# Kernel optimization log

Measured on AMD Instinct MI355X. Metric: run time of the kernel, lower is better.

The kernel has to match this reference:

```python
import jax, jax.numpy as jnp
import numpy as np

HEAD_SIZE = 64
N_EMBD = 1024

def setup_inputs() -> dict:
    key = jax.random.key(0)
    ks = jax.random.split(key, 7)
    B, T = 4, 4096
    s = 1.0 / np.sqrt(N_EMBD)
    return {
        "x": jax.random.normal(ks[0], (B, T, N_EMBD), dtype=jnp.float32),
        "Wq": jax.random.normal(ks[1], (N_EMBD, HEAD_SIZE), dtype=jnp.float32) * s,
        "bq": jnp.zeros((HEAD_SIZE,), dtype=jnp.float32),
        "Wk": jax.random.normal(ks[2], (N_EMBD, HEAD_SIZE), dtype=jnp.float32) * s,
        "bk": jnp.zeros((HEAD_SIZE,), dtype=jnp.float32),
        "Wv": jax.random.normal(ks[3], (N_EMBD, HEAD_SIZE), dtype=jnp.float32) * s,
        "bv": jnp.zeros((HEAD_SIZE,), dtype=jnp.float32),
    }

def reference(x, Wq, bq, Wk, bk, Wv, bv):
    # q,k,v: [B,T,H]
    q = x @ Wq + bq
    k = x @ Wk + bk
    v = x @ Wv + bv
    scale = jnp.asarray(HEAD_SIZE, x.dtype) ** -0.5
    att = jnp.einsum("bth,bsh->bts", q, k) * scale  # [B,T,T]
    att = jax.nn.softmax(att, axis=-1)
    # dropout with p=0.0 is identity (eval-mode reference)
    return jnp.einsum("bts,bsh->bth", att, v)
```

## Files before the change

kernel.cpp:

```cpp
#include <hip/hip_runtime.h>
#include <hip/hip_bf16.h>
#include <cmath>

#define BATCH 4
#define TLEN  4096
#define CEMB  1024
#define HEAD  64
#define NROWS (BATCH * TLEN)

typedef __bf16 bf16;
typedef __attribute__((ext_vector_type(8))) __bf16 bf16x8;
typedef __attribute__((ext_vector_type(4))) __bf16 bf16x4;
typedef __attribute__((ext_vector_type(4))) float f32x4;
typedef __attribute__((ext_vector_type(16))) float f32x16;
typedef __attribute__((ext_vector_type(4))) unsigned u32x4;

#define QSCALE 0.1803368801111204f

static __device__ __forceinline__ f32x4 mfma16(bf16x8 a, bf16x8 b, f32x4 c) {
    return __builtin_amdgcn_mfma_f32_16x16x32_bf16(a, b, c, 0, 0, 0);
}
static __device__ __forceinline__ f32x16 mfma32(bf16x8 a, bf16x8 b, f32x16 c) {
    return __builtin_amdgcn_mfma_f32_32x32x16_bf16(a, b, c, 0, 0, 0);
}
static __device__ __forceinline__ unsigned cvt_pk_bf16(float lo, float hi) {
    unsigned r;
    asm("v_cvt_pk_bf16_f32 %0, %1, %2" : "=v"(r) : "v"(lo), "v"(hi));
    return r;
}

static __device__ __forceinline__ void async_ld16(const void* g, void* l) {
    __builtin_amdgcn_global_load_lds(
        (const __attribute__((address_space(1))) void*)g,
        (__attribute__((address_space(3))) void*)l, 16, 0, 0);
}

__global__ __launch_bounds__(256) void pack_w(
    const float* __restrict__ Wq, const float* __restrict__ Wk,
    const float* __restrict__ Wv, bf16* __restrict__ Wt)
{
    const int n = blockIdx.x;
    const int which = n >> 6, h = n & 63;
    const float* W = which == 0 ? Wq : (which == 1 ? Wk : Wv);
    const float s = which == 0 ? QSCALE : 1.0f;
    for (int k = threadIdx.x; k < CEMB; k += 256)
        Wt[(size_t)n * CEMB + k] = (bf16)(W[(size_t)k * HEAD + h] * s);
}

__global__ __launch_bounds__(256, 2) void qkv(
    const float* __restrict__ x, const bf16* __restrict__ Wt,
    const float* __restrict__ bq, const float* __restrict__ bk,
    const float* __restrict__ bv,
    bf16* __restrict__ qb, bf16* __restrict__ kb, bf16* __restrict__ vT)
{
    __shared__ __align__(16) float Xsh[2][2][32][64];

    const int tid  = threadIdx.x;
    const int lane = tid & 63;
    const int wvid = tid >> 6;
    const int quad = lane >> 4;
    const int col  = lane & 15;
    const int row0 = blockIdx.x * 32;

    const float* xblk = x + (size_t)row0 * CEMB;
    const bf16* wrow[3];
    #pragma unroll
    for (int j = 0; j < 3; ++j)
        wrow[j] = Wt + (size_t)((wvid * 3 + j) * 16 + col) * CEMB + quad * 8;

    const int sr = lane >> 4;
    const int ss = lane & 15;
    auto stage = [&](int ci, int bufi) {
        #pragma unroll
        for (int h2 = 0; h2 < 2; ++h2)
            #pragma unroll
            for (int j = 0; j < 2; ++j) {
                const int r = wvid * 8 + j * 4 + sr;
                const int c = ss ^ (r & 7);
                async_ld16(xblk + (size_t)r * CEMB + ci * 128 + h2 * 64 + c * 4,
                           &Xsh[bufi][h2][wvid * 8 + j * 4][0]);
            }
    };

    f32x4 acc[2][3] = {};
    const int c7 = col & 7;

    stage(0, 0);
    int buf = 0;
    for (int ci = 0; ci < 8; ++ci) {
        __syncthreads();
        if (ci + 1 < 8) stage(ci + 1, buf ^ 1);

        #pragma unroll
        for (int kk = 0; kk < 4; ++kk) {
            const int h  = ci * 4 + kk;
            const int hf = kk >> 1;
            const int kl = kk & 1;
            bf16x8 Bv[3];
            #pragma unroll
            for (int j = 0; j < 3; ++j)
                Bv[j] = *(const bf16x8*)(wrow[j] + h * 32);
            #pragma unroll
            for (int rt = 0; rt < 2; ++rt) {
                const int r = rt * 16 + col;
                const int g0 = kl * 8 + quad * 2;
                float4 a0 = *(const float4*)&Xsh[buf][hf][r][(g0 ^ c7) * 4];
                float4 a1 = *(const float4*)&Xsh[buf][hf][r][((g0 + 1) ^ c7) * 4];
                bf16x8 af;
                af[0]=(bf16)a0.x; af[1]=(bf16)a0.y; af[2]=(bf16)a0.z; af[3]=(bf16)a0.w;
                af[4]=(bf16)a1.x; af[5]=(bf16)a1.y; af[6]=(bf16)a1.z; af[7]=(bf16)a1.w;
                #pragma unroll
                for (int j = 0; j < 3; ++j)
                    acc[rt][j] = mfma16(af, Bv[j], acc[rt][j]);
            }
        }
        buf ^= 1;
    }

    const float* bias[3] = {bq, bk, bv};
    #pragma unroll
    for (int j = 0; j < 3; ++j) {
        const int jg = wvid * 3 + j;
        const int which = jg >> 2;
        const int h = (jg & 3) * 16 + col;
        float bb = bias[which][h];
        if (which == 0) bb *= QSCALE;
        #pragma unroll
        for (int rt = 0; rt < 2; ++rt) {
            if (which < 2) {
                bf16* dst = which == 0 ? qb : kb;
                #pragma unroll
                for (int r = 0; r < 4; ++r) {
                    const int trow = row0 + rt * 16 + quad * 4 + r;
                    dst[(size_t)trow * HEAD + h] = (bf16)(acc[rt][j][r] + bb);
                }
            } else {
                bf16x4 pv;
                #pragma unroll
                for (int r = 0; r < 4; ++r) pv[r] = (bf16)(acc[rt][j][r] + bb);
                const int trow0 = row0 + rt * 16 + quad * 4;
                const int bb_   = trow0 >> 12;
                const int tt    = trow0 & (TLEN - 1);
                *(bf16x4*)(vT + ((size_t)(bb_ * HEAD + h)) * TLEN + tt) = pv;
            }
        }
    }
}

__global__ __launch_bounds__(256, 2) void attn(
    const bf16* __restrict__ qb, const bf16* __restrict__ kb,
    const bf16* __restrict__ vT,
    bf16* __restrict__ opart, float* __restrict__ lpart,
    float* __restrict__ out, int nsplit, int lg2S)
{
    __shared__ __align__(16) bf16 Ksh[2][64][64];
    __shared__ __align__(16) bf16 Vsh[2][64][64];

    const int tid  = threadIdx.x;
    const int lane = tid & 63;
    const int wvid = tid >> 6;
    const int l31  = lane & 31;
    const int b5   = lane >> 5;

    int b, sp, qtile;
    {
        const int id = blockIdx.x;
        if (nsplit >= 2) {
            const int cpx = (BATCH << lg2S) >> 3;
            const int idx = id >> 3;
            const int combo = (id & 7) * cpx + (idx >> 4);
            qtile = idx & 15;
            b = combo >> lg2S;
            sp = combo & (nsplit - 1);
        } else {
            qtile = id & 15; b = id >> 4; sp = 0;
        }
    }
    const int q0 = qtile * 256 + wvid * 64;
    const size_t rowbase = (size_t)b * TLEN + q0;

    bf16x8 qf[2][4];
    #pragma unroll
    for (int qt = 0; qt < 2; ++qt)
        #pragma unroll
        for (int m = 0; m < 4; ++m)
            qf[qt][m] = *(const bf16x8*)
                (qb + (rowbase + qt * 32 + l31) * HEAD + m * 16 + b5 * 8);

    const bf16* kbB = kb + (size_t)b * TLEN * HEAD;
    const bf16* vTB = vT + (size_t)b * HEAD * TLEN;

    f32x16 o[2][2] = {};
    float lsum[2] = {0.f, 0.f};

    const int slen = TLEN >> lg2S;
    const int sbeg = sp * slen;
    const int nch  = slen / 64;

    const int r8 = lane >> 3;
    const int s8 = lane & 7;
    auto stage = [&](int s0, int bufi) {
        #pragma unroll
        for (int j = 0; j < 2; ++j) {
            const int r = wvid * 16 + j * 8 + r8;
            const int c = s8 ^ (r & 7);
            async_ld16(kbB + (size_t)(s0 + r) * HEAD + c * 8,
                       &Ksh[bufi][wvid * 16 + j * 8][0]);
            async_ld16(vTB + (size_t)r * TLEN + s0 + c * 8,
                       &Vsh[bufi][wvid * 16 + j * 8][0]);
        }
    };

    stage(sbeg, 0);
    int buf = 0;
    for (int ci = 0; ci < nch; ++ci) {
        __syncthreads();
        if (ci + 1 < nch) stage(sbeg + (ci + 1) * 64, buf ^ 1);

        #pragma unroll
        for (int kt = 0; kt < 2; ++kt) {
            const int kr = kt * 32 + l31;
            const int k7 = kr & 7;
            bf16x8 kf[4];
            #pragma unroll
            for (int m = 0; m < 4; ++m)
                kf[m] = *(const bf16x8*)&Ksh[buf][kr][((2 * m + b5) ^ k7) * 8];

            bf16x8 pb[2][2];
            #pragma unroll
            for (int qt = 0; qt < 2; ++qt) {
                f32x16 st = {};
                #pragma unroll
                for (int m = 0; m < 4; ++m)
                    st = mfma32(kf[m], qf[qt][m], st);
                float e[16];
                #pragma unroll
                for (int r = 0; r < 16; ++r)
                    e[r] = __builtin_amdgcn_exp2f(st[r]);
                float t0 = (e[0] + e[1]) + (e[2] + e[3]);
                float t1 = (e[4] + e[5]) + (e[6] + e[7]);
                float t2 = (e[8] + e[9]) + (e[10] + e[11]);
                float t3 = (e[12] + e[13]) + (e[14] + e[15]);
                lsum[qt] += (t0 + t1) + (t2 + t3);
                unsigned w[8];
                #pragma unroll
                for (int s = 0; s < 8; ++s)
                    w[s] = cvt_pk_bf16(e[2 * s], e[2 * s + 1]);
                #pragma unroll
                for (int kc = 0; kc < 2; ++kc) {
                    auto s02 = __builtin_amdgcn_permlane32_swap(
                        w[4 * kc + 0], w[4 * kc + 2], false, false);
                    auto s13 = __builtin_amdgcn_permlane32_swap(
                        w[4 * kc + 1], w[4 * kc + 3], false, false);
                    u32x4 pw = { (unsigned)s02[0], (unsigned)s13[0],
                                 (unsigned)s02[1], (unsigned)s13[1] };
                    pb[qt][kc] = __builtin_bit_cast(bf16x8, pw);
                }
            }
            #pragma unroll
            for (int ht = 0; ht < 2; ++ht) {
                const int vr = ht * 32 + l31;
                const int v7 = vr & 7;
                #pragma unroll
                for (int kc = 0; kc < 2; ++kc) {
                    bf16x8 vf = *(const bf16x8*)
                        &Vsh[buf][vr][((2 * (2 * kt + kc) + b5) ^ v7) * 8];
                    #pragma unroll
                    for (int qt = 0; qt < 2; ++qt)
                        o[qt][ht] = mfma32(vf, pb[qt][kc], o[qt][ht]);
                }
            }
        }
        buf ^= 1;
    }

    #pragma unroll
    for (int qt = 0; qt < 2; ++qt)
        lsum[qt] += __shfl_xor(lsum[qt], 32, 64);

    #pragma unroll
    for (int qt = 0; qt < 2; ++qt) {
        const size_t grow = rowbase + qt * 32 + l31;
        if (nsplit == 1) {
            const float inv = 1.f / lsum[qt];
            float* ob = out + grow * HEAD;
            #pragma unroll
            for (int ht = 0; ht < 2; ++ht)
                #pragma unroll
                for (int g = 0; g < 4; ++g) {
                    f32x4 r = { o[qt][ht][4*g+0] * inv, o[qt][ht][4*g+1] * inv,
                                o[qt][ht][4*g+2] * inv, o[qt][ht][4*g+3] * inv };
                    *(f32x4*)(ob + ht * 32 + g * 8 + b5 * 4) = r;
                }
        } else if (sp == 0) {
            float* ob = out + grow * HEAD;
            #pragma unroll
            for (int ht = 0; ht < 2; ++ht)
                #pragma unroll
                for (int g = 0; g < 4; ++g) {
                    f32x4 r = { o[qt][ht][4*g+0], o[qt][ht][4*g+1],
                                o[qt][ht][4*g+2], o[qt][ht][4*g+3] };
                    *(f32x4*)(ob + ht * 32 + g * 8 + b5 * 4) = r;
                }
            if (lane < 32) lpart[grow] = lsum[qt];
        } else {
            bf16* ob = opart + ((size_t)(sp - 1) * NROWS + grow) * HEAD;
            #pragma unroll
            for (int ht = 0; ht < 2; ++ht)
                #pragma unroll
                for (int g = 0; g < 4; ++g) {
                    bf16x4 r = { (bf16)o[qt][ht][4*g+0], (bf16)o[qt][ht][4*g+1],
                                 (bf16)o[qt][ht][4*g+2], (bf16)o[qt][ht][4*g+3] };
                    *(bf16x4*)(ob + ht * 32 + g * 8 + b5 * 4) = r;
                }
            if (lane < 32) lpart[(size_t)sp * NROWS + grow] = lsum[qt];
        }
    }
}

__global__ __launch_bounds__(256) void combine(
    const bf16* __restrict__ opart, const float* __restrict__ lpart,
    float* __restrict__ out, int nsplit)
{
    const int gid = blockIdx.x * 256 + threadIdx.x;
    const int row = gid >> 4;
    const int h4  = (gid & 15) * 4;

    float L = 0.f;
    for (int s = 0; s < nsplit; ++s) L += lpart[(size_t)s * NROWS + row];
    f32x4 O = *(const f32x4*)(out + (size_t)row * HEAD + h4);
    for (int s = 1; s < nsplit; ++s) {
        bf16x4 v = *(const bf16x4*)(opart + ((size_t)(s - 1) * NROWS + row) * HEAD + h4);
        O[0] += (float)v[0]; O[1] += (float)v[1];
        O[2] += (float)v[2]; O[3] += (float)v[3];
    }
    f32x4 r = O * (1.f / L);
    *(f32x4*)(out + (size_t)row * HEAD + h4) = r;
}

extern "C" void kernel_launch(void* const* d_in, const int* in_sizes, int n_in,
                              void* d_out, int out_size, void* d_ws, size_t ws_size,
                              hipStream_t stream) {
    const float* x  = (const float*)d_in[0];
    const float* Wq = (const float*)d_in[1];
    const float* bq = (const float*)d_in[2];
    const float* Wk = (const float*)d_in[3];
    const float* bk = (const float*)d_in[4];
    const float* Wv = (const float*)d_in[5];
    const float* bv = (const float*)d_in[6];
    float* out = (float*)d_out;

    const size_t n_tok = (size_t)NROWS * HEAD;
    char* ws = (char*)d_ws;
    bf16* qb = (bf16*)ws;
    bf16* kb = qb + n_tok;
    bf16* vT = kb + n_tok;
    bf16* Wt = vT + n_tok;
    const size_t base = 3 * n_tok * sizeof(bf16) + 192 * CEMB * sizeof(bf16);

    auto need = [&](int S) {
        return base + (size_t)(S - 1) * n_tok * sizeof(bf16)
                    + (size_t)S * NROWS * sizeof(float);
    };
    int S = 1, lg2S = 0;
    if      (ws_size >= need(8)) { S = 8; lg2S = 3; }
    else if (ws_size >= need(4)) { S = 4; lg2S = 2; }
    else if (ws_size >= need(2)) { S = 2; lg2S = 1; }
    bf16*  opart = Wt + 192 * CEMB;
    float* lpart = (float*)(opart + (size_t)(S - 1) * n_tok);

    pack_w<<<dim3(192), dim3(256), 0, stream>>>(Wq, Wk, Wv, Wt);
    qkv<<<dim3(512), dim3(256), 0, stream>>>(x, Wt, bq, bk, bv, qb, kb, vT);
    attn<<<dim3(16 * BATCH * S), dim3(256), 0, stream>>>(
        qb, kb, vT, opart, lpart, out, S, lg2S);
    if (S > 1)
        combine<<<dim3((NROWS * 16) / 256), dim3(256), 0, stream>>>(
            opart, lpart, out, S);
}
```

Measured before the change: 159.2 us.

## Pre-swizzle packed weights into MFMA fragment order and load x directly

The weight packing kernel now stages W tiles through shared memory and writes bf16 weights in the exact per-lane MFMA fragment layout, so each lane's B operand load in the QKV projection is one contiguous 16-byte read. The projection kernel drops its double-buffered async LDS staging of x and instead reads x rows straight from global memory into registers before converting to bf16. This removes LDS traffic and barriers in the projection, and makes the pack kernel's reads coalesced. The tradeoff is less coalesced global x reads, since each lane strides by a full row, with no explicit prefetch overlap.

```diff
diff --git a/kernel.cpp b/kernel.cpp
--- a/kernel.cpp
+++ b/kernel.cpp
@@ -39,12 +39,37 @@
     const float* __restrict__ Wq, const float* __restrict__ Wk,
     const float* __restrict__ Wv, bf16* __restrict__ Wt)
 {
-    const int n = blockIdx.x;
-    const int which = n >> 6, h = n & 63;
+    __shared__ float Wl[128][68];
+    const int which = blockIdx.x >> 3;
+    const int kb    = blockIdx.x & 7;
+    const int t     = threadIdx.x;
     const float* W = which == 0 ? Wq : (which == 1 ? Wk : Wv);
     const float s = which == 0 ? QSCALE : 1.0f;
-    for (int k = threadIdx.x; k < CEMB; k += 256)
-        Wt[(size_t)n * CEMB + k] = (bf16)(W[(size_t)k * HEAD + h] * s);
+
+    const float4* Wf = (const float4*)(W + (size_t)kb * 128 * 64);
+    #pragma unroll
+    for (int i = 0; i < 8; ++i) {
+        const int f = i * 256 + t;
+        float4 w = Wf[f];
+        *(float4*)&Wl[f >> 4][(f & 15) * 4] = w;
+    }
+    __syncthreads();
+
+    const int lanex = t & 63;
+    const int grp   = t >> 6;
+    const int quad  = lanex >> 4, colx = lanex & 15;
+    #pragma unroll
+    for (int it = 0; it < 4; ++it) {
+        const int seg = it * 4 + grp;
+        const int jg4 = seg >> 2, h4 = seg & 3;
+        bf16x8 o;
+        #pragma unroll
+        for (int e = 0; e < 8; ++e)
+            o[e] = (bf16)(Wl[h4 * 32 + quad * 8 + e][jg4 * 16 + colx] * s);
+        const int jg = which * 4 + jg4;
+        const int h  = kb * 4 + h4;
+        *(bf16x8*)(Wt + ((size_t)(jg * 32 + h) * 64 + lanex) * 8) = o;
+    }
 }
 
 __global__ __launch_bounds__(256, 2) void qkv(
@@ -53,8 +78,6 @@
     const float* __restrict__ bv,
     bf16* __restrict__ qb, bf16* __restrict__ kb, bf16* __restrict__ vT)
 {
-    __shared__ __align__(16) float Xsh[2][2][32][64];
-
     const int tid  = threadIdx.x;
     const int lane = tid & 63;
     const int wvid = tid >> 6;
@@ -62,59 +85,32 @@
     const int col  = lane & 15;
     const int row0 = blockIdx.x * 32;
 
-    const float* xblk = x + (size_t)row0 * CEMB;
-    const bf16* wrow[3];
+    const bf16* wbase[3];
     #pragma unroll
     for (int j = 0; j < 3; ++j)
-        wrow[j] = Wt + (size_t)((wvid * 3 + j) * 16 + col) * CEMB + quad * 8;
-
-    const int sr = lane >> 4;
-    const int ss = lane & 15;
-    auto stage = [&](int ci, int bufi) {
-        #pragma unroll
-        for (int h2 = 0; h2 < 2; ++h2)
-            #pragma unroll
-            for (int j = 0; j < 2; ++j) {
-                const int r = wvid * 8 + j * 4 + sr;
-                const int c = ss ^ (r & 7);
-                async_ld16(xblk + (size_t)r * CEMB + ci * 128 + h2 * 64 + c * 4,
-                           &Xsh[bufi][h2][wvid * 8 + j * 4][0]);
-            }
-    };
+        wbase[j] = Wt + (size_t)(wvid * 3 + j) * 32 * 64 * 8 + (size_t)lane * 8;
+    const float* xb0 = x + (size_t)(row0 + col) * CEMB + quad * 8;
+    const float* xb1 = xb0 + (size_t)16 * CEMB;
 
     f32x4 acc[2][3] = {};
-    const int c7 = col & 7;
-
-    stage(0, 0);
-    int buf = 0;
-    for (int ci = 0; ci < 8; ++ci) {
-        __syncthreads();
-        if (ci + 1 < 8) stage(ci + 1, buf ^ 1);
-
-        #pragma unroll
-        for (int kk = 0; kk < 4; ++kk) {
-            const int h  = ci * 4 + kk;
-            const int hf = kk >> 1;
-            const int kl = kk & 1;
-            bf16x8 Bv[3];
+    #pragma unroll 8
+    for (int h = 0; h < 32; ++h) {
+        bf16x8 Bv[3];
+        #pragma unroll
+        for (int j = 0; j < 3; ++j)
+            Bv[j] = *(const bf16x8*)(wbase[j] + (size_t)h * 512);
+        #pragma unroll
+        for (int rt = 0; rt < 2; ++rt) {
+            const float* xp = (rt ? xb1 : xb0) + h * 32;
+            float4 a0 = *(const float4*)xp;
+            float4 a1 = *(const float4*)(xp + 4);
+            bf16x8 af;
+            af[0]=(bf16)a0.x; af[1]=(bf16)a0.y; af[2]=(bf16)a0.z; af[3]=(bf16)a0.w;
+            af[4]=(bf16)a1.x; af[5]=(bf16)a1.y; af[6]=(bf16)a1.z; af[7]=(bf16)a1.w;
             #pragma unroll
             for (int j = 0; j < 3; ++j)
-                Bv[j] = *(const bf16x8*)(wrow[j] + h * 32);
-            #pragma unroll
-            for (int rt = 0; rt < 2; ++rt) {
-                const int r = rt * 16 + col;
-                const int g0 = kl * 8 + quad * 2;
-                float4 a0 = *(const float4*)&Xsh[buf][hf][r][(g0 ^ c7) * 4];
-                float4 a1 = *(const float4*)&Xsh[buf][hf][r][((g0 + 1) ^ c7) * 4];
-                bf16x8 af;
-                af[0]=(bf16)a0.x; af[1]=(bf16)a0.y; af[2]=(bf16)a0.z; af[3]=(bf16)a0.w;
-                af[4]=(bf16)a1.x; af[5]=(bf16)a1.y; af[6]=(bf16)a1.z; af[7]=(bf16)a1.w;
-                #pragma unroll
-                for (int j = 0; j < 3; ++j)
-                    acc[rt][j] = mfma16(af, Bv[j], acc[rt][j]);
-            }
-        }
-        buf ^= 1;
+                acc[rt][j] = mfma16(af, Bv[j], acc[rt][j]);
+        }
     }
 
     const float* bias[3] = {bq, bk, bv};
@@ -369,7 +365,7 @@
     bf16*  opart = Wt + 192 * CEMB;
     float* lpart = (float*)(opart + (size_t)(S - 1) * n_tok);
 
-    pack_w<<<dim3(192), dim3(256), 0, stream>>>(Wq, Wk, Wv, Wt);
+    pack_w<<<dim3(24), dim3(256), 0, stream>>>(Wq, Wk, Wv, Wt);
     qkv<<<dim3(512), dim3(256), 0, stream>>>(x, Wt, bq, bk, bv, qb, kb, vT);
     attn<<<dim3(16 * BATCH * S), dim3(256), 0, stream>>>(
         qb, kb, vT, opart, lpart, out, S, lg2S);
```

Result: slower. 172.6 us (+8.5%).
